# Kernel optimization log

Hardware: AMD Instinct MI355X
Metric: run time of the kernel (lower is better)

## Reference

```python
import jax, jax.numpy as jnp
import numpy as np

DIM = 1024
MULT = 4
HID = DIM * MULT
E = 8
B, S = 2, 2048


def _rmsnorm(x):
    # zeta SimpleRMSNorm: F.normalize(x, dim=-1) * sqrt(dim)
    n = jnp.linalg.norm(x, axis=-1, keepdims=True)
    return x / jnp.maximum(n, 1e-12) * jnp.sqrt(jnp.asarray(x.shape[-1], x.dtype))


def _act_quant(x):
    # per-token 8-bit absmax quant (BitNet b1.58), straight-through in fwd math
    scale = 127.0 / jnp.clip(jnp.max(jnp.abs(x), axis=-1, keepdims=True), 1e-5)
    q = jnp.clip(jnp.round(x * scale), -128, 127) / scale
    return x + jax.lax.stop_gradient(q - x)


def _w_quant(w, axes):
    # ternary weight quant with per-matrix mean-abs scale
    scale = 1.0 / jnp.clip(jnp.mean(jnp.abs(w), axis=axes, keepdims=True), 1e-5)
    q = jnp.clip(jnp.round(w * scale), -1, 1) / scale
    return w + jax.lax.stop_gradient(q - w)


def setup_inputs() -> dict:
    key = jax.random.key(0)
    ks = jax.random.split(key, 8)
    sd = 0.02
    x = jax.random.normal(ks[0], (B, S, DIM), dtype=jnp.float32)
    gw = jax.random.normal(ks[1], (E, DIM), dtype=jnp.float32) * sd
    gb = jnp.zeros((E,), dtype=jnp.float32)
    w1 = jax.random.normal(ks[2], (E, HID, DIM), dtype=jnp.float32) * sd
    b1 = jnp.zeros((E, HID), dtype=jnp.float32)
    w2 = jax.random.normal(ks[3], (E, DIM, HID), dtype=jnp.float32) * sd
    b2 = jnp.zeros((E, DIM), dtype=jnp.float32)
    return {"x": x, "gw": gw, "gb": gb, "w1": w1, "b1": b1, "w2": w2, "b2": b2}


def reference(x, gw, gb, w1, b1, w2, b2):
    # BitLinear input preprocessing: RMSNorm then 8-bit activation quant
    xq = _act_quant(_rmsnorm(x))  # [B,S,D]

    # Gate: softmax(BitLinear(dim, E))
    logits = jnp.einsum("bsd,ed->bse", xq, _w_quant(gw, axes=(0, 1))) + gb
    gates = jax.nn.softmax(logits, axis=-1)  # [B,S,E]

    # Experts: BitLinear -> GELU -> BitLinear, quant scales per expert
    w1q = _w_quant(w1, axes=(1, 2))  # [E,H,D]
    w2q = _w_quant(w2, axes=(1, 2))  # [E,D,H]
    h = jnp.einsum("bsd,ehd->bseh", xq, w1q) + b1  # [B,S,E,H]
    a = jax.nn.gelu(h, approximate=False)
    aq = _act_quant(_rmsnorm(a))
    expert_out = jnp.einsum("bseh,edh->bsed", aq, w2q) + b2  # [B,S,E,D]

    # softmax-weighted sum over experts
    return jnp.einsum("bse,bsed->bsd", gates, expert_out)
```

## Files before the change

### kernel.cpp

```cpp
#include <hip/hip_runtime.h>


#define T_TOK 4096
#define DIMS  1024
#define HID   4096
#define NE    8
#define ROWB  8192ull

typedef __attribute__((ext_vector_type(4))) int       i32x4;
typedef __attribute__((ext_vector_type(8))) _Float16  f16x8;

__device__ __forceinline__ float block_sum(float v, float* buf, int tid) {
  #pragma unroll
  for (int o = 32; o > 0; o >>= 1) v += __shfl_down(v, o, 64);
  __syncthreads();
  if ((tid & 63) == 0) buf[tid >> 6] = v;
  __syncthreads();
  return buf[0] + buf[1] + buf[2] + buf[3];
}
__device__ __forceinline__ float block_max(float v, float* buf, int tid) {
  #pragma unroll
  for (int o = 32; o > 0; o >>= 1) { float t = __shfl_down(v, o, 64); v = fmaxf(v, t); }
  __syncthreads();
  if ((tid & 63) == 0) buf[tid >> 6] = v;
  __syncthreads();
  return fmaxf(fmaxf(buf[0], buf[1]), fmaxf(buf[2], buf[3]));
}

__device__ __forceinline__ void gl_lds16(const void* g, void* l) {
  __builtin_amdgcn_global_load_lds(
      (const __attribute__((address_space(1))) unsigned int*)g,
      (__attribute__((address_space(3))) unsigned int*)l, 16, 0, 0);
}

__device__ __forceinline__ int q8(float v) {
  return ((int)fminf(fmaxf(rintf(v), -128.0f), 127.0f)) & 0xff;
}

__device__ __forceinline__ float erf_fast(float x) {
  const float ax = fabsf(x);
  const float t = __builtin_amdgcn_rcpf(fmaf(0.3275911f, ax, 1.0f));
  float p = fmaf(1.061405429f, t, -1.453152027f);
  p = fmaf(p, t, 1.421413741f);
  p = fmaf(p, t, -0.284496736f);
  p = fmaf(p, t, 0.254829592f);
  p = p * t;
  const float e = __expf(-ax * ax);
  const float r = fmaf(-p, e, 1.0f);
  return copysignf(r, x);
}
__device__ __forceinline__ float gelu_fast(float h) {
  return 0.5f * h * (1.0f + erf_fast(h * 0.70710678118654752f));
}

__device__ __forceinline__ const i32x4* frag(const char* s, int row, int ckW) {
  return (const i32x4*)&s[row * 128 + ((ckW ^ (row & 7)) << 4)];
}

__global__ __launch_bounds__(256) void wabs_sum_kernel(
    const float4* __restrict__ w, int n_f4, int shift, float* __restrict__ sums) {
  __shared__ float buf[4];
  const int tid = threadIdx.x;
  const int base = blockIdx.x * 4096;
  float acc = 0.0f;
  for (int k = 0; k < 16; ++k) {
    int fi = base + k * 256 + tid;
    if (fi < n_f4) {
      float4 v = w[fi];
      acc += fabsf(v.x) + fabsf(v.y) + fabsf(v.z) + fabsf(v.w);
    }
  }
  acc = block_sum(acc, buf, tid);
  if (tid == 0) atomicAdd(&sums[base >> shift], acc);
}

__global__ void mkscales_kernel(const float* __restrict__ wsum, float* __restrict__ sc) {
  if (threadIdx.x == 0) {
    #pragma unroll
    for (int e = 0; e < NE; ++e) {
      float m1 = fmaxf(wsum[e] * (1.0f / 4194304.0f), 1e-5f);
      sc[e] = m1; sc[8 + e] = 1.0f / m1;
      float m2 = fmaxf(wsum[8 + e] * (1.0f / 4194304.0f), 1e-5f);
      sc[16 + e] = m2; sc[24 + e] = 1.0f / m2;
    }
    float mg = fmaxf(wsum[16] * (1.0f / 8192.0f), 1e-5f);
    sc[32] = mg; sc[33] = 1.0f / mg;
  }
}

__global__ __launch_bounds__(256) void wquant_kernel(
    const float4* __restrict__ w, int* __restrict__ o, int n_f4, int shift,
    const float* __restrict__ qs) {
  int fi = blockIdx.x * 256 + threadIdx.x;
  if (fi >= n_f4) return;
  const float s = qs[fi >> shift];
  float4 v = w[fi];
  int b0 = ((int)fminf(fmaxf(rintf(v.x * s), -1.0f), 1.0f)) & 0xff;
  int b1 = ((int)fminf(fmaxf(rintf(v.y * s), -1.0f), 1.0f)) & 0xff;
  int b2 = ((int)fminf(fmaxf(rintf(v.z * s), -1.0f), 1.0f)) & 0xff;
  int b3 = ((int)fminf(fmaxf(rintf(v.w * s), -1.0f), 1.0f)) & 0xff;
  o[fi] = b0 | (b1 << 8) | (b2 << 16) | (b3 << 24);
}

__global__ __launch_bounds__(256) void preprocess_kernel(
    const float* __restrict__ x, const float* __restrict__ gw,
    const float* __restrict__ gb, const float* __restrict__ scales,
    int* __restrict__ qx, float* __restrict__ inv_sx, float* __restrict__ gates) {
  __shared__ float buf[4];
  const int t = blockIdx.x, tid = threadIdx.x;
  const float4 xv = ((const float4*)(x + (size_t)t * DIMS))[tid];
  float ss = xv.x * xv.x + xv.y * xv.y + xv.z * xv.z + xv.w * xv.w;
  ss = block_sum(ss, buf, tid);
  const float rr = 32.0f / fmaxf(sqrtf(ss), 1e-12f);
  const float y0 = xv.x * rr, y1 = xv.y * rr, y2 = xv.z * rr, y3 = xv.w * rr;
  float am = fmaxf(fmaxf(fabsf(y0), fabsf(y1)), fmaxf(fabsf(y2), fabsf(y3)));
  am = block_max(am, buf, tid);
  const float aclip = fmaxf(am, 1e-5f);
  const float qsc = 127.0f / aclip;
  const float q0 = fminf(fmaxf(rintf(y0 * qsc), -128.0f), 127.0f);
  const float q1 = fminf(fmaxf(rintf(y1 * qsc), -128.0f), 127.0f);
  const float q2 = fminf(fmaxf(rintf(y2 * qsc), -128.0f), 127.0f);
  const float q3 = fminf(fmaxf(rintf(y3 * qsc), -128.0f), 127.0f);
  qx[t * 256 + tid] = (((int)q0) & 0xff) | ((((int)q1) & 0xff) << 8) |
                      ((((int)q2) & 0xff) << 16) | ((((int)q3) & 0xff) << 24);

  const float gsabs = scales[32], gqs = scales[33];
  float lg[NE];
  #pragma unroll
  for (int e = 0; e < NE; ++e) {
    const float4 gv = ((const float4*)(gw + e * DIMS))[tid];
    float t0 = fminf(fmaxf(rintf(gv.x * gqs), -1.0f), 1.0f);
    float t1 = fminf(fmaxf(rintf(gv.y * gqs), -1.0f), 1.0f);
    float t2 = fminf(fmaxf(rintf(gv.z * gqs), -1.0f), 1.0f);
    float t3 = fminf(fmaxf(rintf(gv.w * gqs), -1.0f), 1.0f);
    lg[e] = q0 * t0 + q1 * t1 + q2 * t2 + q3 * t3;
  }
  #pragma unroll
  for (int e = 0; e < NE; ++e) lg[e] = block_sum(lg[e], buf, tid);
  if (tid == 0) {
    const float isx = aclip / 127.0f;
    inv_sx[t] = isx;
    float l[NE], mx = -1e30f;
    #pragma unroll
    for (int e = 0; e < NE; ++e) { l[e] = lg[e] * (isx * gsabs) + gb[e]; mx = fmaxf(mx, l[e]); }
    float s = 0.0f;
    #pragma unroll
    for (int e = 0; e < NE; ++e) { l[e] = expf(l[e] - mx); s += l[e]; }
    const float inv = 1.0f / s;
    #pragma unroll
    for (int e = 0; e < NE; ++e) gates[t * NE + e] = l[e] * inv;
  }
}

__global__ __launch_bounds__(256, 2) void gemm1_kernel(
    const char* __restrict__ qx, const char* __restrict__ w1q,
    const float* __restrict__ scales, const float* __restrict__ inv_sx,
    const float* __restrict__ b1, char* __restrict__ aqa) {
  __shared__ __align__(16) char sA[256 * 128];
  __shared__ __align__(16) char sB[128 * 128];
  const int e = blockIdx.z;
  const char* A = qx;
  const char* Bm = w1q + (size_t)e * HID * DIMS;
  char* obase = aqa + (size_t)e * T_TOK * ROWB;
  const int n0 = blockIdx.x * 128, m0 = blockIdx.y * 256;
  const int tid = threadIdx.x, lane = tid & 63, wv = tid >> 6;
  const int wr = (wv >> 1) * 128, wc = (wv & 1) * 64, lm = lane & 15, lq = lane >> 4;
  i32x4 acc[8][4] = {};
  for (int k0 = 0; k0 < DIMS; k0 += 128) {
    #pragma unroll
    for (int it = 0; it < 8; ++it) {
      const int c = it * 256 + tid;
      const int row = c >> 3, ckG = (c & 7) ^ (row & 7);
      gl_lds16(A + (size_t)(m0 + row) * DIMS + k0 + ckG * 16, &sA[c * 16]);
    }
    #pragma unroll
    for (int it = 0; it < 4; ++it) {
      const int c = it * 256 + tid;
      const int row = c >> 3, ckG = (c & 7) ^ (row & 7);
      gl_lds16(Bm + (size_t)(n0 + row) * DIMS + k0 + ckG * 16, &sB[c * 16]);
    }
    __syncthreads();
    #pragma unroll
    for (int kk = 0; kk < 2; ++kk) {
      i32x4 av[8], bv[4];
      const int ckW = kk * 4 + lq;
      #pragma unroll
      for (int i = 0; i < 8; ++i) av[i] = *frag(sA, wr + i * 16 + lm, ckW);
      #pragma unroll
      for (int j = 0; j < 4; ++j) bv[j] = *frag(sB, wc + j * 16 + lm, ckW);
      #pragma unroll
      for (int i = 0; i < 8; ++i)
        #pragma unroll
        for (int j = 0; j < 4; ++j)
          acc[i][j] = __builtin_amdgcn_mfma_i32_16x16x64_i8(av[i], bv[j], acc[i][j], 0, 0, 0);
    }
    __syncthreads();
  }
  const float s1 = scales[e];
  float bb[4];
  #pragma unroll
  for (int j = 0; j < 4; ++j) bb[j] = b1[e * HID + n0 + wc + j * 16 + lm];
  #pragma unroll
  for (int i = 0; i < 8; ++i) {
    #pragma unroll
    for (int r = 0; r < 4; ++r) {
      const int row = m0 + wr + i * 16 + lq * 4 + r;
      const float rs = inv_sx[row] * s1;
      _Float16* orow = (_Float16*)(obase + (size_t)row * ROWB);
      #pragma unroll
      for (int j = 0; j < 4; ++j) {
        const int col = n0 + wc + j * 16 + lm;
        orow[col] = (_Float16)fmaf((float)acc[i][j][r], rs, bb[j]);
      }
    }
  }
}

__global__ __launch_bounds__(256) void rowquant_kernel(
    char* __restrict__ aqa, float* __restrict__ inv_sa) {
  __shared__ float buf[4];
  const size_t R = blockIdx.x;
  char* rowb = aqa + R * ROWB;
  const int tid = threadIdx.x;
  f16x8 v0 = ((const f16x8*)rowb)[tid * 2];
  f16x8 v1 = ((const f16x8*)rowb)[tid * 2 + 1];
  float f[16];
  #pragma unroll
  for (int k = 0; k < 8; ++k) { f[k] = (float)v0[k]; f[8 + k] = (float)v1[k]; }
  #pragma unroll
  for (int k = 0; k < 16; ++k) f[k] = gelu_fast(f[k]);
  float ss = 0.0f;
  #pragma unroll
  for (int k = 0; k < 16; ++k) ss += f[k] * f[k];
  ss = block_sum(ss, buf, tid);
  const float rr = 64.0f / fmaxf(sqrtf(ss), 1e-12f);
  float am = 0.0f;
  #pragma unroll
  for (int k = 0; k < 16; ++k) am = fmaxf(am, fabsf(f[k] * rr));
  am = block_max(am, buf, tid);
  const float aclip = fmaxf(am, 1e-5f);
  const float qsc = rr * 127.0f / aclip;
  int4 o;
  o.x = q8(f[0] * qsc) | (q8(f[1] * qsc) << 8) | (q8(f[2] * qsc) << 16) | (q8(f[3] * qsc) << 24);
  o.y = q8(f[4] * qsc) | (q8(f[5] * qsc) << 8) | (q8(f[6] * qsc) << 16) | (q8(f[7] * qsc) << 24);
  o.z = q8(f[8] * qsc) | (q8(f[9] * qsc) << 8) | (q8(f[10] * qsc) << 16) | (q8(f[11] * qsc) << 24);
  o.w = q8(f[12] * qsc) | (q8(f[13] * qsc) << 8) | (q8(f[14] * qsc) << 16) | (q8(f[15] * qsc) << 24);
  ((int4*)rowb)[tid] = o;
  if (tid == 0) inv_sa[R] = aclip / 127.0f;
}

__global__ __launch_bounds__(256, 2) void gemm2_kernel(
    const char* __restrict__ aqa, const char* __restrict__ w2q,
    const float* __restrict__ scales, const float* __restrict__ inv_sa,
    const float* __restrict__ b2, const float* __restrict__ gates,
    void* __restrict__ dstv, int use_atomic) {
  __shared__ __align__(16) char sA[256 * 128];
  __shared__ __align__(16) char sB[128 * 128];
  const int e = blockIdx.z;
  const char* A = aqa + (size_t)e * T_TOK * ROWB;
  const char* Bm = w2q + (size_t)e * DIMS * HID;
  const int n0 = blockIdx.x * 128, m0 = blockIdx.y * 256;
  const int tid = threadIdx.x, lane = tid & 63, wv = tid >> 6;
  const int wr = (wv >> 1) * 128, wc = (wv & 1) * 64, lm = lane & 15, lq = lane >> 4;
  i32x4 acc[8][4] = {};
  for (int k0 = 0; k0 < HID; k0 += 128) {
    #pragma unroll
    for (int it = 0; it < 8; ++it) {
      const int c = it * 256 + tid;
      const int row = c >> 3, ckG = (c & 7) ^ (row & 7);
      gl_lds16(A + (size_t)(m0 + row) * ROWB + k0 + ckG * 16, &sA[c * 16]);
    }
    #pragma unroll
    for (int it = 0; it < 4; ++it) {
      const int c = it * 256 + tid;
      const int row = c >> 3, ckG = (c & 7) ^ (row & 7);
      gl_lds16(Bm + (size_t)(n0 + row) * HID + k0 + ckG * 16, &sB[c * 16]);
    }
    __syncthreads();
    #pragma unroll
    for (int kk = 0; kk < 2; ++kk) {
      i32x4 av[8], bv[4];
      const int ckW = kk * 4 + lq;
      #pragma unroll
      for (int i = 0; i < 8; ++i) av[i] = *frag(sA, wr + i * 16 + lm, ckW);
      #pragma unroll
      for (int j = 0; j < 4; ++j) bv[j] = *frag(sB, wc + j * 16 + lm, ckW);
      #pragma unroll
      for (int i = 0; i < 8; ++i)
        #pragma unroll
        for (int j = 0; j < 4; ++j)
          acc[i][j] = __builtin_amdgcn_mfma_i32_16x16x64_i8(av[i], bv[j], acc[i][j], 0, 0, 0);
    }
    __syncthreads();
  }
  const float s2 = scales[16 + e];
  float bb[4];
  #pragma unroll
  for (int j = 0; j < 4; ++j) bb[j] = b2[e * DIMS + n0 + wc + j * 16 + lm];
  #pragma unroll
  for (int i = 0; i < 8; ++i) {
    #pragma unroll
    for (int r = 0; r < 4; ++r) {
      const int row = m0 + wr + i * 16 + lq * 4 + r;
      const float rs = inv_sa[(size_t)e * T_TOK + row] * s2;
      const float g = gates[row * NE + e];
      #pragma unroll
      for (int j = 0; j < 4; ++j) {
        const int col = n0 + wc + j * 16 + lm;
        const float v = g * fmaf((float)acc[i][j][r], rs, bb[j]);
        if (use_atomic) atomicAdd(&((float*)dstv)[(size_t)row * DIMS + col], v);
        else ((_Float16*)dstv)[((size_t)e * T_TOK + row) * DIMS + col] = (_Float16)v;
      }
    }
  }
}

__global__ __launch_bounds__(256) void reduce_kernel(
    const f16x8* __restrict__ eout, float4* __restrict__ out) {
  const int i = blockIdx.x * 256 + threadIdx.x;
  float s[8] = {};
  #pragma unroll
  for (int e = 0; e < NE; ++e) {
    f16x8 v = eout[(size_t)e * (T_TOK * DIMS / 8) + i];
    #pragma unroll
    for (int k = 0; k < 8; ++k) s[k] += (float)v[k];
  }
  float4 o0; o0.x = s[0]; o0.y = s[1]; o0.z = s[2]; o0.w = s[3];
  float4 o1; o1.x = s[4]; o1.y = s[5]; o1.z = s[6]; o1.w = s[7];
  out[i * 2]     = o0;
  out[i * 2 + 1] = o1;
}

extern "C" void kernel_launch(void* const* d_in, const int* in_sizes, int n_in,
                              void* d_out, int out_size, void* d_ws, size_t ws_size,
                              hipStream_t stream) {
  const float* x  = (const float*)d_in[0];
  const float* gw = (const float*)d_in[1];
  const float* gb = (const float*)d_in[2];
  const float* w1 = (const float*)d_in[3];
  const float* b1 = (const float*)d_in[4];
  const float* w2 = (const float*)d_in[5];
  const float* b2 = (const float*)d_in[6];
  float* outp = (float*)d_out;
  char* ws = (char*)d_ws;

  float* wsum   = (float*)(ws + 0);
  float* scales = (float*)(ws + 256);
  float* inv_sx = (float*)(ws + 4096);
  float* gates  = (float*)(ws + 20480);
  float* inv_sa = (float*)(ws + 151552);
  char*  qx     = ws + 282624;
  char*  w1q    = ws + 4476928;
  char*  w2q    = ws + 38031360;
  char*  aqa    = ws + 71585792;
  char*  eout   = ws + 340021248;

  const bool has_eout = ws_size >= 340021248ull + 67108864ull;

  hipMemsetAsync(wsum, 0, 17 * sizeof(float), stream);
  wabs_sum_kernel<<<2048, 256, 0, stream>>>((const float4*)w1, 8388608, 20, wsum + 0);
  wabs_sum_kernel<<<2048, 256, 0, stream>>>((const float4*)w2, 8388608, 20, wsum + 8);
  wabs_sum_kernel<<<1,    256, 0, stream>>>((const float4*)gw, 2048,    30, wsum + 16);
  mkscales_kernel<<<1, 64, 0, stream>>>(wsum, scales);
  wquant_kernel<<<32768, 256, 0, stream>>>((const float4*)w1, (int*)w1q, 8388608, 20, scales + 8);
  wquant_kernel<<<32768, 256, 0, stream>>>((const float4*)w2, (int*)w2q, 8388608, 20, scales + 24);
  preprocess_kernel<<<4096, 256, 0, stream>>>(x, gw, gb, scales, (int*)qx, inv_sx, gates);

  gemm1_kernel<<<dim3(32, 16, 8), 256, 0, stream>>>(qx, w1q, scales, inv_sx, b1, aqa);
  rowquant_kernel<<<32768, 256, 0, stream>>>(aqa, inv_sa);

  if (has_eout) {
    gemm2_kernel<<<dim3(8, 16, 8), 256, 0, stream>>>(
        aqa, w2q, scales, inv_sa, b2, gates, eout, 0);
    reduce_kernel<<<2048, 256, 0, stream>>>((const f16x8*)eout, (float4*)outp);
  } else {
    hipMemsetAsync(outp, 0, (size_t)out_size * sizeof(float), stream);
    gemm2_kernel<<<dim3(8, 16, 8), 256, 0, stream>>>(
        aqa, w2q, scales, inv_sa, b2, gates, outp, 1);
  }
}
```

Baseline: 890.5 us.

## Rewrite int8 expert GEMMs with 4-stage async LDS pipeline and 256x256 tiles

Both expert GEMMs now share one int8 MFMA core. It uses 512-thread blocks, 256x256 output tiles and a 4-deep ring of 64-wide K slices in LDS, with loads issued three stages ahead and synchronised through vmcnt waits and raw barriers. The grid is flattened so the expert index varies fastest, which spreads experts across CUs. The aim is to hide global-to-LDS latency behind MFMA work and raise reuse per tile. In exchange, LDS use per block is large (128 KB), which may limit occupancy, and the hand-written waitcnt logic is fragile.

```diff
diff --git a/kernel.cpp b/kernel.cpp
--- a/kernel.cpp
+++ b/kernel.cpp
@@ -51,10 +51,6 @@
 }
 __device__ __forceinline__ float gelu_fast(float h) {
   return 0.5f * h * (1.0f + erf_fast(h * 0.70710678118654752f));
-}
-
-__device__ __forceinline__ const i32x4* frag(const char* s, int row, int ckW) {
-  return (const i32x4*)&s[row * 128 + ((ckW ^ (row & 7)) << 4)];
 }
 
 __global__ __launch_bounds__(256) void wabs_sum_kernel(
@@ -124,7 +120,7 @@
   qx[t * 256 + tid] = (((int)q0) & 0xff) | ((((int)q1) & 0xff) << 8) |
                       ((((int)q2) & 0xff) << 16) | ((((int)q3) & 0xff) << 24);
 
-  const float gsabs = scales[32], gqs = scales[33];
+  const float gqs = scales[33];
   float lg[NE];
   #pragma unroll
   for (int e = 0; e < NE; ++e) {
@@ -138,6 +134,7 @@
   #pragma unroll
   for (int e = 0; e < NE; ++e) lg[e] = block_sum(lg[e], buf, tid);
   if (tid == 0) {
+    const float gsabs = scales[32];
     const float isx = aclip / 127.0f;
     inv_sx[t] = isx;
     float l[NE], mx = -1e30f;
@@ -152,50 +149,90 @@
   }
 }
 
-__global__ __launch_bounds__(256, 2) void gemm1_kernel(
+template <int SA, int SB, int NT>
+__device__ __forceinline__ void gemm_core_i8(
+    const char* __restrict__ A, const char* __restrict__ Bm,
+    int m0, int n0, char* sA, char* sB, i32x4 (&acc)[8][4]) {
+  const int tid = threadIdx.x;
+  const int lane = tid & 63;
+  const int lm = lane & 15, lq = lane >> 4;
+  const int wv = tid >> 6;
+  const int wr = (wv >> 2) * 128, wc = (wv & 3) * 64;
+
+  const int c0 = tid, c1 = 512 + tid;
+  const int r0 = c0 >> 2, r1 = c1 >> 2;
+  const int g0 = ((c0 & 3) ^ ((r0 >> 1) & 3)) << 4;
+  const int g1 = ((c1 & 3) ^ ((r1 >> 1) & 3)) << 4;
+  const char* gA0 = A + (size_t)(m0 + r0) * SA + g0;
+  const char* gA1 = A + (size_t)(m0 + r1) * SA + g1;
+  const char* gB0 = Bm + (size_t)(n0 + r0) * SB + g0;
+  const char* gB1 = Bm + (size_t)(n0 + r1) * SB + g1;
+  const int l0 = c0 * 16, l1 = c1 * 16;
+
+  const int swz = (lq ^ ((lm >> 1) & 3)) << 4;
+  const int aoff = (wr + lm) * 64 + swz;
+  const int boff = (wc + lm) * 64 + swz;
+
+#define STAGE_I8(j)                                           \
+  do {                                                        \
+    const int _b = (j) & 3; const int _k = (j) * 64;          \
+    gl_lds16(gA0 + _k, sA + _b * 16384 + l0);                 \
+    gl_lds16(gA1 + _k, sA + _b * 16384 + l1);                 \
+    gl_lds16(gB0 + _k, sB + _b * 16384 + l0);                 \
+    gl_lds16(gB1 + _k, sB + _b * 16384 + l1);                 \
+  } while (0)
+
+  STAGE_I8(0); STAGE_I8(1); STAGE_I8(2);
+  asm volatile("s_waitcnt vmcnt(8)" ::: "memory");
+  __builtin_amdgcn_s_barrier();
+  asm volatile("" ::: "memory");
+
+  for (int t = 0; t < NT; ++t) {
+    const int cur = t & 3;
+    if (t + 3 < NT) STAGE_I8(t + 3);
+    const char* bA = sA + cur * 16384;
+    const char* bB = sB + cur * 16384;
+    i32x4 av[8], bv[4];
+    #pragma unroll
+    for (int i = 0; i < 8; ++i) av[i] = *(const i32x4*)(bA + aoff + i * 1024);
+    #pragma unroll
+    for (int j = 0; j < 4; ++j) bv[j] = *(const i32x4*)(bB + boff + j * 1024);
+    __builtin_amdgcn_s_setprio(1);
+    #pragma unroll
+    for (int i = 0; i < 8; ++i)
+      #pragma unroll
+      for (int j = 0; j < 4; ++j)
+        acc[i][j] = __builtin_amdgcn_mfma_i32_16x16x64_i8(av[i], bv[j], acc[i][j], 0, 0, 0);
+    __builtin_amdgcn_s_setprio(0);
+    if (t < NT - 1) {
+      if (t + 3 < NT)       { asm volatile("s_waitcnt vmcnt(8)" ::: "memory"); }
+      else if (t + 3 == NT) { asm volatile("s_waitcnt vmcnt(4)" ::: "memory"); }
+      else                  { asm volatile("s_waitcnt vmcnt(0)" ::: "memory"); }
+      __builtin_amdgcn_s_barrier();
+      asm volatile("" ::: "memory");
+    }
+  }
+#undef STAGE_I8
+}
+
+__global__ __launch_bounds__(512, 2) void gemm1_kernel(
     const char* __restrict__ qx, const char* __restrict__ w1q,
     const float* __restrict__ scales, const float* __restrict__ inv_sx,
     const float* __restrict__ b1, char* __restrict__ aqa) {
-  __shared__ __align__(16) char sA[256 * 128];
-  __shared__ __align__(16) char sB[128 * 128];
-  const int e = blockIdx.z;
-  const char* A = qx;
+  __shared__ __align__(16) char sA[4 * 16384];
+  __shared__ __align__(16) char sB[4 * 16384];
+  const int wg = blockIdx.x;
+  const int e = wg & 7;
+  const int i2 = wg >> 3;
+  const int yi = i2 & 15, xi = i2 >> 4;
+  const int m0 = yi * 256, n0 = xi * 256;
   const char* Bm = w1q + (size_t)e * HID * DIMS;
+  i32x4 acc[8][4] = {};
+  gemm_core_i8<DIMS, DIMS, DIMS / 64>(qx, Bm, m0, n0, sA, sB, acc);
+
+  const int tid = threadIdx.x, lane = tid & 63, wv = tid >> 6;
+  const int wr = (wv >> 2) * 128, wc = (wv & 3) * 64, lm = lane & 15, lq = lane >> 4;
   char* obase = aqa + (size_t)e * T_TOK * ROWB;
-  const int n0 = blockIdx.x * 128, m0 = blockIdx.y * 256;
-  const int tid = threadIdx.x, lane = tid & 63, wv = tid >> 6;
-  const int wr = (wv >> 1) * 128, wc = (wv & 1) * 64, lm = lane & 15, lq = lane >> 4;
-  i32x4 acc[8][4] = {};
-  for (int k0 = 0; k0 < DIMS; k0 += 128) {
-    #pragma unroll
-    for (int it = 0; it < 8; ++it) {
-      const int c = it * 256 + tid;
-      const int row = c >> 3, ckG = (c & 7) ^ (row & 7);
-      gl_lds16(A + (size_t)(m0 + row) * DIMS + k0 + ckG * 16, &sA[c * 16]);
-    }
-    #pragma unroll
-    for (int it = 0; it < 4; ++it) {
-      const int c = it * 256 + tid;
-      const int row = c >> 3, ckG = (c & 7) ^ (row & 7);
-      gl_lds16(Bm + (size_t)(n0 + row) * DIMS + k0 + ckG * 16, &sB[c * 16]);
-    }
-    __syncthreads();
-    #pragma unroll
-    for (int kk = 0; kk < 2; ++kk) {
-      i32x4 av[8], bv[4];
-      const int ckW = kk * 4 + lq;
-      #pragma unroll
-      for (int i = 0; i < 8; ++i) av[i] = *frag(sA, wr + i * 16 + lm, ckW);
-      #pragma unroll
-      for (int j = 0; j < 4; ++j) bv[j] = *frag(sB, wc + j * 16 + lm, ckW);
-      #pragma unroll
-      for (int i = 0; i < 8; ++i)
-        #pragma unroll
-        for (int j = 0; j < 4; ++j)
-          acc[i][j] = __builtin_amdgcn_mfma_i32_16x16x64_i8(av[i], bv[j], acc[i][j], 0, 0, 0);
-    }
-    __syncthreads();
-  }
   const float s1 = scales[e];
   float bb[4];
   #pragma unroll
@@ -249,50 +286,25 @@
   if (tid == 0) inv_sa[R] = aclip / 127.0f;
 }
 
-__global__ __launch_bounds__(256, 2) void gemm2_kernel(
+__global__ __launch_bounds__(512, 2) void gemm2_kernel(
     const char* __restrict__ aqa, const char* __restrict__ w2q,
     const float* __restrict__ scales, const float* __restrict__ inv_sa,
     const float* __restrict__ b2, const float* __restrict__ gates,
     void* __restrict__ dstv, int use_atomic) {
-  __shared__ __align__(16) char sA[256 * 128];
-  __shared__ __align__(16) char sB[128 * 128];
-  const int e = blockIdx.z;
+  __shared__ __align__(16) char sA[4 * 16384];
+  __shared__ __align__(16) char sB[4 * 16384];
+  const int wg = blockIdx.x;
+  const int e = wg & 7;
+  const int i2 = wg >> 3;
+  const int xi = i2 & 3, yi = i2 >> 2;
+  const int m0 = yi * 256, n0 = xi * 256;
   const char* A = aqa + (size_t)e * T_TOK * ROWB;
   const char* Bm = w2q + (size_t)e * DIMS * HID;
-  const int n0 = blockIdx.x * 128, m0 = blockIdx.y * 256;
+  i32x4 acc[8][4] = {};
+  gemm_core_i8<(int)ROWB, HID, HID / 64>(A, Bm, m0, n0, sA, sB, acc);
+
   const int tid = threadIdx.x, lane = tid & 63, wv = tid >> 6;
-  const int wr = (wv >> 1) * 128, wc = (wv & 1) * 64, lm = lane & 15, lq = lane >> 4;
-  i32x4 acc[8][4] = {};
-  for (int k0 = 0; k0 < HID; k0 += 128) {
-    #pragma unroll
-    for (int it = 0; it < 8; ++it) {
-      const int c = it * 256 + tid;
-      const int row = c >> 3, ckG = (c & 7) ^ (row & 7);
-      gl_lds16(A + (size_t)(m0 + row) * ROWB + k0 + ckG * 16, &sA[c * 16]);
-    }
-    #pragma unroll
-    for (int it = 0; it < 4; ++it) {
-      const int c = it * 256 + tid;
-      const int row = c >> 3, ckG = (c & 7) ^ (row & 7);
-      gl_lds16(Bm + (size_t)(n0 + row) * HID + k0 + ckG * 16, &sB[c * 16]);
-    }
-    __syncthreads();
-    #pragma unroll
-    for (int kk = 0; kk < 2; ++kk) {
-      i32x4 av[8], bv[4];
-      const int ckW = kk * 4 + lq;
-      #pragma unroll
-      for (int i = 0; i < 8; ++i) av[i] = *frag(sA, wr + i * 16 + lm, ckW);
-      #pragma unroll
-      for (int j = 0; j < 4; ++j) bv[j] = *frag(sB, wc + j * 16 + lm, ckW);
-      #pragma unroll
-      for (int i = 0; i < 8; ++i)
-        #pragma unroll
-        for (int j = 0; j < 4; ++j)
-          acc[i][j] = __builtin_amdgcn_mfma_i32_16x16x64_i8(av[i], bv[j], acc[i][j], 0, 0, 0);
-    }
-    __syncthreads();
-  }
+  const int wr = (wv >> 2) * 128, wc = (wv & 3) * 64, lm = lane & 15, lq = lane >> 4;
   const float s2 = scales[16 + e];
   float bb[4];
   #pragma unroll
@@ -366,16 +378,16 @@
   wquant_kernel<<<32768, 256, 0, stream>>>((const float4*)w2, (int*)w2q, 8388608, 20, scales + 24);
   preprocess_kernel<<<4096, 256, 0, stream>>>(x, gw, gb, scales, (int*)qx, inv_sx, gates);
 
-  gemm1_kernel<<<dim3(32, 16, 8), 256, 0, stream>>>(qx, w1q, scales, inv_sx, b1, aqa);
+  gemm1_kernel<<<2048, 512, 0, stream>>>(qx, w1q, scales, inv_sx, b1, aqa);
   rowquant_kernel<<<32768, 256, 0, stream>>>(aqa, inv_sa);
 
   if (has_eout) {
-    gemm2_kernel<<<dim3(8, 16, 8), 256, 0, stream>>>(
+    gemm2_kernel<<<512, 512, 0, stream>>>(
         aqa, w2q, scales, inv_sa, b2, gates, eout, 0);
     reduce_kernel<<<2048, 256, 0, stream>>>((const f16x8*)eout, (float4*)outp);
   } else {
     hipMemsetAsync(outp, 0, (size_t)out_size * sizeof(float), stream);
-    gemm2_kernel<<<dim3(8, 16, 8), 256, 0, stream>>>(
+    gemm2_kernel<<<512, 512, 0, stream>>>(
         aqa, w2q, scales, inv_sa, b2, gates, outp, 1);
   }
 }
```

Result: slower. 938.2 us (+5.4%).

## Remap GEMM workgroups so each XCD handles one expert, add nontemporal stores

Applied to the files above, without the earlier changes.

Flattens the 3D grids of both expert GEMMs into 1D and derives the expert index from the low 3 bits of the block id, so round-robin dispatch across XCDs keeps each expert's weights and tiles within one XCD's L2. The tile traversal order inside each expert also changes. Output stores of the 16-bit intermediates become nontemporal to avoid polluting cache with streaming data. This risks losing cache hits when the next kernel reads those intermediates.

```diff
diff --git a/kernel.cpp b/kernel.cpp
--- a/kernel.cpp
+++ b/kernel.cpp
@@ -124,7 +124,7 @@
   qx[t * 256 + tid] = (((int)q0) & 0xff) | ((((int)q1) & 0xff) << 8) |
                       ((((int)q2) & 0xff) << 16) | ((((int)q3) & 0xff) << 24);
 
-  const float gsabs = scales[32], gqs = scales[33];
+  const float gqs = scales[33];
   float lg[NE];
   #pragma unroll
   for (int e = 0; e < NE; ++e) {
@@ -138,6 +138,7 @@
   #pragma unroll
   for (int e = 0; e < NE; ++e) lg[e] = block_sum(lg[e], buf, tid);
   if (tid == 0) {
+    const float gsabs = scales[32];
     const float isx = aclip / 127.0f;
     inv_sx[t] = isx;
     float l[NE], mx = -1e30f;
@@ -158,11 +159,14 @@
     const float* __restrict__ b1, char* __restrict__ aqa) {
   __shared__ __align__(16) char sA[256 * 128];
   __shared__ __align__(16) char sB[128 * 128];
-  const int e = blockIdx.z;
+  const int wg = blockIdx.x;
+  const int e = wg & 7;
+  const int i2 = wg >> 3;
+  const int yi = i2 & 15, xi = i2 >> 4;
+  const int n0 = xi * 128, m0 = yi * 256;
   const char* A = qx;
   const char* Bm = w1q + (size_t)e * HID * DIMS;
   char* obase = aqa + (size_t)e * T_TOK * ROWB;
-  const int n0 = blockIdx.x * 128, m0 = blockIdx.y * 256;
   const int tid = threadIdx.x, lane = tid & 63, wv = tid >> 6;
   const int wr = (wv >> 1) * 128, wc = (wv & 1) * 64, lm = lane & 15, lq = lane >> 4;
   i32x4 acc[8][4] = {};
@@ -210,7 +214,8 @@
       #pragma unroll
       for (int j = 0; j < 4; ++j) {
         const int col = n0 + wc + j * 16 + lm;
-        orow[col] = (_Float16)fmaf((float)acc[i][j][r], rs, bb[j]);
+        __builtin_nontemporal_store((_Float16)fmaf((float)acc[i][j][r], rs, bb[j]),
+                                    &orow[col]);
       }
     }
   }
@@ -256,10 +261,13 @@
     void* __restrict__ dstv, int use_atomic) {
   __shared__ __align__(16) char sA[256 * 128];
   __shared__ __align__(16) char sB[128 * 128];
-  const int e = blockIdx.z;
+  const int wg = blockIdx.x;
+  const int e = wg & 7;
+  const int i2 = wg >> 3;
+  const int xi = i2 & 7, yi = i2 >> 3;
+  const int n0 = xi * 128, m0 = yi * 256;
   const char* A = aqa + (size_t)e * T_TOK * ROWB;
   const char* Bm = w2q + (size_t)e * DIMS * HID;
-  const int n0 = blockIdx.x * 128, m0 = blockIdx.y * 256;
   const int tid = threadIdx.x, lane = tid & 63, wv = tid >> 6;
   const int wr = (wv >> 1) * 128, wc = (wv & 1) * 64, lm = lane & 15, lq = lane >> 4;
   i32x4 acc[8][4] = {};
@@ -309,7 +317,9 @@
         const int col = n0 + wc + j * 16 + lm;
         const float v = g * fmaf((float)acc[i][j][r], rs, bb[j]);
         if (use_atomic) atomicAdd(&((float*)dstv)[(size_t)row * DIMS + col], v);
-        else ((_Float16*)dstv)[((size_t)e * T_TOK + row) * DIMS + col] = (_Float16)v;
+        else __builtin_nontemporal_store(
+                 (_Float16)v,
+                 &((_Float16*)dstv)[((size_t)e * T_TOK + row) * DIMS + col]);
       }
     }
   }
@@ -366,16 +376,16 @@
   wquant_kernel<<<32768, 256, 0, stream>>>((const float4*)w2, (int*)w2q, 8388608, 20, scales + 24);
   preprocess_kernel<<<4096, 256, 0, stream>>>(x, gw, gb, scales, (int*)qx, inv_sx, gates);
 
-  gemm1_kernel<<<dim3(32, 16, 8), 256, 0, stream>>>(qx, w1q, scales, inv_sx, b1, aqa);
+  gemm1_kernel<<<4096, 256, 0, stream>>>(qx, w1q, scales, inv_sx, b1, aqa);
   rowquant_kernel<<<32768, 256, 0, stream>>>(aqa, inv_sa);
 
   if (has_eout) {
-    gemm2_kernel<<<dim3(8, 16, 8), 256, 0, stream>>>(
+    gemm2_kernel<<<1024, 256, 0, stream>>>(
         aqa, w2q, scales, inv_sa, b2, gates, eout, 0);
     reduce_kernel<<<2048, 256, 0, stream>>>((const f16x8*)eout, (float4*)outp);
   } else {
     hipMemsetAsync(outp, 0, (size_t)out_size * sizeof(float), stream);
-    gemm2_kernel<<<dim3(8, 16, 8), 256, 0, stream>>>(
+    gemm2_kernel<<<1024, 256, 0, stream>>>(
         aqa, w2q, scales, inv_sa, b2, gates, outp, 1);
   }
 }
```

New measurement: 891.9 us. No clear change (+0.2%).
